# Kernel tuning notes

Measured on AMD Instinct MI355X. Metric: run time of the kernel, lower is better.

## Reference

```python
import jax, jax.numpy as jnp
import numpy as np
from jax import lax

# Matches init_kwargs: ops='co', window_size=[51, 25]
OPS = "co"
WINDOWS = [51, 25]


def _stage(x, k, mode):
    # Torch Conv1d(padding='same') zero-pads left=(k-1)//2, right=k//2, and the
    # identity-shift kernel bank + channel min/max is exactly a sliding-window
    # min/max over the zero-padded signal.
    left, right = (k - 1) // 2, k // 2
    xp = jnp.pad(x, ((0, 0), (0, 0), (left, right)))  # zeros, as in torch 'same'
    if mode == "max":  # dilation
        return lax.reduce_window(xp, float("-inf"), lax.max, (1, 1, k), (1, 1, 1), "VALID")
    # erosion
    return lax.reduce_window(xp, float("inf"), lax.min, (1, 1, k), (1, 1, 1), "VALID")


def _chain(x):
    # Per-channel python loop in the original is channel-independent; we batch it.
    for op, k in zip(OPS, WINDOWS):
        if op.lower() == "c":  # closing: dilation then erosion
            x = _stage(x, k, "max")
            x = _stage(x, k, "min")
        elif op.lower() == "o":  # opening: erosion then dilation
            x = _stage(x, k, "min")
            x = _stage(x, k, "max")
    return x


def setup_inputs() -> dict:
    key = jax.random.key(0)
    x = jax.random.normal(key, (16, 8, 262144), dtype=jnp.float32)  # [B, C, L]
    return {"x": x}


def reference(x):
    return _chain(x)
```

## Files before the change

### kernel.cpp

```cpp
#include <hip/hip_runtime.h>


#define L_ROW   262144
#define N_ROWS  128
#define BLOCK   256
#define E       32
#define EF4     8
#define T_VALID 7996
#define N_TILES 33
#define BUF_SLOTS 2048

__device__ __forceinline__ int swz(int s) { return s ^ ((s >> 3) & 7); }

template<bool MX>
__device__ __forceinline__ float mm(float a, float b) {
  return MX ? fmaxf(a, b) : fminf(a, b);
}

__device__ __forceinline__ void edge_zero(float* r, int goff, int tid, bool edge) {
  if (edge) {
    const int base = goff + tid * E;
#pragma unroll
    for (int i = 0; i < E; ++i)
      if ((unsigned)(base + i) >= (unsigned)L_ROW) r[i] = 0.0f;
  }
}

__device__ __forceinline__ void writeback(const float* r, float4* buf, int b4) {
#pragma unroll
  for (int j = 0; j < EF4; ++j)
    buf[swz(b4 + j)] = make_float4(r[4*j], r[4*j+1], r[4*j+2], r[4*j+3]);
  __syncthreads();
}

template<int K, bool MX>
__device__ __forceinline__ void stage_big(float* r, float4* buf, int tid,
                                          int goff, bool edge) {
  constexpr int BLEN = K - 33;
  constexpr int BN   = (BLEN + 2) / 4;
  const int b4 = tid * EF4;
  const int bh = min(b4, 2032 - BN);

  float4 v0 = buf[swz(bh + 8)];
  float a0 = v0.x, a1 = v0.y, a2 = v0.z, a3 = v0.w;
#pragma unroll
  for (int j = 1; j < BN - 1; ++j) {
    float4 v = buf[swz(bh + 8 + j)];
    a0 = mm<MX>(a0, v.x); a1 = mm<MX>(a1, v.y);
    a2 = mm<MX>(a2, v.z); a3 = mm<MX>(a3, v.w);
  }
  float4 vl = buf[swz(bh + 8 + BN - 1)];
  const float Base = mm<MX>(mm<MX>(mm<MX>(a0, a1), mm<MX>(a2, a3)),
                            mm<MX>(vl.x, vl.y));
  float T[34];
  T[0] = vl.z; T[1] = vl.w;
#pragma unroll
  for (int j = 0; j < 8; ++j) {
    float4 v = buf[swz(bh + 8 + BN + j)];
    T[2+4*j] = v.x; T[3+4*j] = v.y; T[4+4*j] = v.z; T[5+4*j] = v.w;
  }
  __syncthreads();

#pragma unroll
  for (int b = 0; b < 4; ++b)
#pragma unroll
    for (int i = 8*b + 6; i >= 8*b; --i) r[i] = mm<MX>(r[i], r[i+1]);
  const float S2 = r[24];
  const float S1 = mm<MX>(r[16], S2);
  const float S0 = mm<MX>(r[8],  S1);
#pragma unroll
  for (int i = 0;  i < 8;  ++i) r[i] = mm<MX>(r[i], S0);
#pragma unroll
  for (int i = 8;  i < 16; ++i) r[i] = mm<MX>(r[i], S1);
#pragma unroll
  for (int i = 16; i < 24; ++i) r[i] = mm<MX>(r[i], S2);

#pragma unroll
  for (int b = 0; b < 4; ++b)
#pragma unroll
    for (int i = 8*b + 1; i < 8*b + 8; ++i) T[i] = mm<MX>(T[i-1], T[i]);
  const float G0 = mm<MX>(Base, T[7]);
  const float G1 = mm<MX>(G0,   T[15]);
  const float G2 = mm<MX>(G1,   T[23]);

#pragma unroll
  for (int i = 0;  i < 8;  ++i) r[i] = mm<MX>(r[i], mm<MX>(Base, T[i]));
#pragma unroll
  for (int i = 8;  i < 16; ++i) r[i] = mm<MX>(r[i], mm<MX>(G0, T[i]));
#pragma unroll
  for (int i = 16; i < 24; ++i) r[i] = mm<MX>(r[i], mm<MX>(G1, T[i]));
#pragma unroll
  for (int i = 24; i < 32; ++i) r[i] = mm<MX>(r[i], mm<MX>(G2, T[i]));

  edge_zero(r, goff, tid, edge);
  writeback(r, buf, b4);
}

template<bool MX>
__device__ __forceinline__ void stage_25(float* r, float4* buf, int tid,
                                         int goff, bool edge) {
  const int b4 = tid * EF4;
  const int bh = min(b4, 2034);
  float h[24];
#pragma unroll
  for (int j = 0; j < 6; ++j) {
    float4 v = buf[swz(bh + 8 + j)];
    h[4*j] = v.x; h[4*j+1] = v.y; h[4*j+2] = v.z; h[4*j+3] = v.w;
  }
  __syncthreads();

  float t[8];
  t[0] = r[24];
#pragma unroll
  for (int i = 1; i < 8; ++i) t[i] = mm<MX>(t[i-1], r[24+i]);
#pragma unroll
  for (int i = 30; i >= 24; --i) r[i] = mm<MX>(r[i], r[i+1]);
#pragma unroll
  for (int i = 22; i >= 16; --i) r[i] = mm<MX>(r[i], r[i+1]);
  const float cA = r[16];
  const float A3 = r[24];
#pragma unroll
  for (int i = 16; i < 24; ++i) r[i] = mm<MX>(r[i], A3);
#pragma unroll
  for (int i = 14; i >= 8; --i) r[i] = mm<MX>(r[i], r[i+1]);
#pragma unroll
  for (int i = 6;  i >= 0; --i) r[i] = mm<MX>(r[i], r[i+1]);
  const float A1 = r[8];
#pragma unroll
  for (int i = 0; i < 8; ++i) r[i] = mm<MX>(r[i], A1);
#pragma unroll
  for (int b = 0; b < 3; ++b)
#pragma unroll
    for (int i = 8*b + 1; i < 8*b + 8; ++i) h[i] = mm<MX>(h[i-1], h[i]);
  const float aB  = h[7];
  const float cA2 = mm<MX>(cA, t[7]);
  const float G1  = mm<MX>(aB, h[15]);
#pragma unroll
  for (int i = 0;  i < 8;  ++i) r[i] = mm<MX>(r[i], mm<MX>(cA,  t[i]));
#pragma unroll
  for (int i = 8;  i < 16; ++i) r[i] = mm<MX>(r[i], mm<MX>(cA2, h[i-8]));
#pragma unroll
  for (int i = 16; i < 24; ++i) r[i] = mm<MX>(r[i], mm<MX>(aB,  h[i-8]));
#pragma unroll
  for (int i = 24; i < 32; ++i) r[i] = mm<MX>(r[i], mm<MX>(G1,  h[i-8]));

  edge_zero(r, goff, tid, edge);
  writeback(r, buf, b4);
}

__global__ __launch_bounds__(BLOCK)
void morph_co_kernel(const float* __restrict__ x, float* __restrict__ out) {
  __shared__ float4 buf[BUF_SLOTS];

  const int tid  = threadIdx.x;
  const int tile = blockIdx.x;
  const int row  = blockIdx.y;
  const float* __restrict__ xrow = x   + (size_t)row * L_ROW;
  float* __restrict__       orow = out + (size_t)row * L_ROW;

  const int c0 = tile * T_VALID - 76;
  const bool edge = (tile == 0) || (tile == N_TILES - 1);

  if (!edge) {
#if __has_builtin(__builtin_amdgcn_global_load_lds)
    const int w = tid >> 6, lane = tid & 63;
#pragma unroll
    for (int k = 0; k < 8; ++k) {
      const int q0 = k * 256 + w * 64;
      const float* g = xrow + c0 + 4 * swz(q0 + lane);
      __builtin_amdgcn_global_load_lds(
          (const __attribute__((address_space(1))) void*)g,
          (__attribute__((address_space(3))) void*)(&buf[q0]), 16, 0, 0);
    }
#else
#pragma unroll
    for (int k = 0; k < 8; ++k) {
      const int s = k * BLOCK + tid;
      buf[swz(s)] = *reinterpret_cast<const float4*>(xrow + c0 + 4 * s);
    }
#endif
  } else {
#pragma unroll
    for (int k = 0; k < 8; ++k) {
      const int s = k * BLOCK + tid;
      const int g = c0 + 4 * s;
      float4 v;
      if (g >= 0 && g + 3 < L_ROW) {
        v = *reinterpret_cast<const float4*>(xrow + g);
      } else {
        v.x = ((unsigned)(g + 0) < (unsigned)L_ROW) ? xrow[g + 0] : 0.0f;
        v.y = ((unsigned)(g + 1) < (unsigned)L_ROW) ? xrow[g + 1] : 0.0f;
        v.z = ((unsigned)(g + 2) < (unsigned)L_ROW) ? xrow[g + 2] : 0.0f;
        v.w = ((unsigned)(g + 3) < (unsigned)L_ROW) ? xrow[g + 3] : 0.0f;
      }
      buf[swz(s)] = v;
    }
  }
  __syncthreads();

  float r[E];
  {
    const int b4 = tid * EF4;
#pragma unroll
    for (int j = 0; j < EF4; ++j) {
      float4 v = buf[swz(b4 + j)];
      r[4*j] = v.x; r[4*j+1] = v.y; r[4*j+2] = v.z; r[4*j+3] = v.w;
    }
  }

  if (!edge) {
    stage_big<51, true >(r, buf, tid, 0, false);
    stage_big<75, false>(r, buf, tid, 0, false);
    stage_25 <     true>(r, buf, tid, 0, false);
  } else {
    stage_big<51, true >(r, buf, tid, c0 + 25, true);
    stage_big<51, false>(r, buf, tid, c0 + 50, true);
    stage_25 <    false>(r, buf, tid, c0 + 62, true);
    stage_25 <     true>(r, buf, tid, c0 + 74, true);
  }

  const int ob  = tile * T_VALID;
  const int nf4 = min(T_VALID, L_ROW - ob) >> 2;
  float4* og = reinterpret_cast<float4*>(orow + ob);
  for (int u = tid; u < nf4; u += BLOCK) {
    float4 a = buf[swz(u)];
    float4 b = buf[swz(u + 1)];
    og[u] = make_float4(a.z, a.w, b.x, b.y);
  }
}

extern "C" void kernel_launch(void* const* d_in, const int* in_sizes, int n_in,
                              void* d_out, int out_size, void* d_ws, size_t ws_size,
                              hipStream_t stream) {
  const float* x = (const float*)d_in[0];
  float* out = (float*)d_out;
  dim3 grid(N_TILES, N_ROWS);
  morph_co_kernel<<<grid, BLOCK, 0, stream>>>(x, out);
}
```

Measured before the change: 51.88 us.

## Give each wavefront its own tile to replace block barriers with wave-local fences

The kernel now splits each row into 135 smaller chunks and assigns one per wavefront, each with a private LDS slice. Because a wavefront's LDS accesses execute in order, the block-wide __syncthreads calls can become compiler-only memory fences and a vmcnt wait, removing barrier stalls between the morphology stages. The trade-off is more halo overlap, since each 1944-sample chunk re-reads about 76 samples on each side, which adds global traffic to an already bandwidth-heavy kernel. Interior outputs are written as unaligned float2 pairs, so neighbouring chunks write some boundary elements twice with identical values.

Measured after the change: 49.25 us, median of 2. -5.1%, faster.

```diff
diff --git a/kernel.cpp b/kernel.cpp
--- a/kernel.cpp
+++ b/kernel.cpp
@@ -6,20 +6,24 @@
 #define BLOCK   256
 #define E       32
 #define EF4     8
-#define T_VALID 7996
-#define N_TILES 33
-#define BUF_SLOTS 2048
+#define T_W     1944
+#define N_CHUNKS 135
+#define NSLOT   528
+
+typedef float f32x2 __attribute__((ext_vector_type(2)));
 
 __device__ __forceinline__ int swz(int s) { return s ^ ((s >> 3) & 7); }
+
+#define WFENCE() asm volatile("" ::: "memory")
 
 template<bool MX>
 __device__ __forceinline__ float mm(float a, float b) {
   return MX ? fmaxf(a, b) : fminf(a, b);
 }
 
-__device__ __forceinline__ void edge_zero(float* r, int goff, int tid, bool edge) {
+__device__ __forceinline__ void edge_zero(float* r, int goff, int lane, bool edge) {
   if (edge) {
-    const int base = goff + tid * E;
+    const int base = goff + lane * E;
 #pragma unroll
     for (int i = 0; i < E; ++i)
       if ((unsigned)(base + i) >= (unsigned)L_ROW) r[i] = 0.0f;
@@ -27,19 +31,20 @@
 }
 
 __device__ __forceinline__ void writeback(const float* r, float4* buf, int b4) {
+  WFENCE();
 #pragma unroll
   for (int j = 0; j < EF4; ++j)
     buf[swz(b4 + j)] = make_float4(r[4*j], r[4*j+1], r[4*j+2], r[4*j+3]);
-  __syncthreads();
+  WFENCE();
 }
 
 template<int K, bool MX>
-__device__ __forceinline__ void stage_big(float* r, float4* buf, int tid,
+__device__ __forceinline__ void stage_big(float* r, float4* buf, int lane,
                                           int goff, bool edge) {
   constexpr int BLEN = K - 33;
   constexpr int BN   = (BLEN + 2) / 4;
-  const int b4 = tid * EF4;
-  const int bh = min(b4, 2032 - BN);
+  const int b4 = lane * EF4;
+  const int bh = min(b4, NSLOT - 16 - BN);
 
   float4 v0 = buf[swz(bh + 8)];
   float a0 = v0.x, a1 = v0.y, a2 = v0.z, a3 = v0.w;
@@ -59,7 +64,6 @@
     float4 v = buf[swz(bh + 8 + BN + j)];
     T[2+4*j] = v.x; T[3+4*j] = v.y; T[4+4*j] = v.z; T[5+4*j] = v.w;
   }
-  __syncthreads();
 
 #pragma unroll
   for (int b = 0; b < 4; ++b)
@@ -92,22 +96,20 @@
 #pragma unroll
   for (int i = 24; i < 32; ++i) r[i] = mm<MX>(r[i], mm<MX>(G2, T[i]));
 
-  edge_zero(r, goff, tid, edge);
+  edge_zero(r, goff, lane, edge);
   writeback(r, buf, b4);
 }
 
 template<bool MX>
-__device__ __forceinline__ void stage_25(float* r, float4* buf, int tid,
+__device__ __forceinline__ void stage_25(float* r, float4* buf, int lane,
                                          int goff, bool edge) {
-  const int b4 = tid * EF4;
-  const int bh = min(b4, 2034);
+  const int b4 = lane * EF4;
   float h[24];
 #pragma unroll
   for (int j = 0; j < 6; ++j) {
-    float4 v = buf[swz(bh + 8 + j)];
+    float4 v = buf[swz(b4 + 8 + j)];
     h[4*j] = v.x; h[4*j+1] = v.y; h[4*j+2] = v.z; h[4*j+3] = v.w;
   }
-  __syncthreads();
 
   float t[8];
   t[0] = r[24];
@@ -144,88 +146,101 @@
 #pragma unroll
   for (int i = 24; i < 32; ++i) r[i] = mm<MX>(r[i], mm<MX>(G1,  h[i-8]));
 
-  edge_zero(r, goff, tid, edge);
+  edge_zero(r, goff, lane, edge);
   writeback(r, buf, b4);
 }
 
 __global__ __launch_bounds__(BLOCK)
 void morph_co_kernel(const float* __restrict__ x, float* __restrict__ out) {
-  __shared__ float4 buf[BUF_SLOTS];
-
-  const int tid  = threadIdx.x;
-  const int tile = blockIdx.x;
+  __shared__ float4 lds4[4 * NSLOT];
+
+  const int w    = threadIdx.x >> 6;
+  const int lane = threadIdx.x & 63;
+  const int c    = blockIdx.x * 4 + w;
   const int row  = blockIdx.y;
+  if (c >= N_CHUNKS) return;
+
+  float4* buf = lds4 + w * NSLOT;
   const float* __restrict__ xrow = x   + (size_t)row * L_ROW;
   float* __restrict__       orow = out + (size_t)row * L_ROW;
 
-  const int c0 = tile * T_VALID - 76;
-  const bool edge = (tile == 0) || (tile == N_TILES - 1);
+  const int ob = c * T_W;
+  const int c0 = ob - 76;
+  const bool edge = (c == 0) || (c == N_CHUNKS - 1);
+  const int b4 = lane * EF4;
+  float r[E];
 
   if (!edge) {
-#if __has_builtin(__builtin_amdgcn_global_load_lds)
-    const int w = tid >> 6, lane = tid & 63;
-#pragma unroll
-    for (int k = 0; k < 8; ++k) {
-      const int q0 = k * 256 + w * 64;
-      const float* g = xrow + c0 + 4 * swz(q0 + lane);
-      __builtin_amdgcn_global_load_lds(
-          (const __attribute__((address_space(1))) void*)g,
-          (__attribute__((address_space(3))) void*)(&buf[q0]), 16, 0, 0);
-    }
-#else
-#pragma unroll
-    for (int k = 0; k < 8; ++k) {
-      const int s = k * BLOCK + tid;
-      buf[swz(s)] = *reinterpret_cast<const float4*>(xrow + c0 + 4 * s);
-    }
-#endif
+#pragma unroll
+    for (int it = 0; it < 9; ++it) {
+      const int s = it * 64 + lane;
+      if (s < NSLOT) {
+        const float* g = xrow + c0 + 4 * swz(s);
+        __builtin_amdgcn_global_load_lds(
+            (const __attribute__((address_space(1))) void*)g,
+            (__attribute__((address_space(3))) void*)(&buf[it * 64]), 16, 0, 0);
+      }
+    }
+    asm volatile("s_waitcnt vmcnt(0)" ::: "memory");
   } else {
 #pragma unroll
-    for (int k = 0; k < 8; ++k) {
-      const int s = k * BLOCK + tid;
-      const int g = c0 + 4 * s;
-      float4 v;
-      if (g >= 0 && g + 3 < L_ROW) {
-        v = *reinterpret_cast<const float4*>(xrow + g);
-      } else {
+    for (int it = 0; it < 9; ++it) {
+      const int s = it * 64 + lane;
+      if (s < NSLOT) {
+        const int g = c0 + 4 * s;
+        float4 v;
         v.x = ((unsigned)(g + 0) < (unsigned)L_ROW) ? xrow[g + 0] : 0.0f;
         v.y = ((unsigned)(g + 1) < (unsigned)L_ROW) ? xrow[g + 1] : 0.0f;
         v.z = ((unsigned)(g + 2) < (unsigned)L_ROW) ? xrow[g + 2] : 0.0f;
         v.w = ((unsigned)(g + 3) < (unsigned)L_ROW) ? xrow[g + 3] : 0.0f;
-      }
-      buf[swz(s)] = v;
-    }
-  }
-  __syncthreads();
-
-  float r[E];
-  {
-    const int b4 = tid * EF4;
-#pragma unroll
-    for (int j = 0; j < EF4; ++j) {
-      float4 v = buf[swz(b4 + j)];
-      r[4*j] = v.x; r[4*j+1] = v.y; r[4*j+2] = v.z; r[4*j+3] = v.w;
-    }
+        buf[swz(s)] = v;
+      }
+    }
+    WFENCE();
+  }
+
+#pragma unroll
+  for (int j = 0; j < EF4; ++j) {
+    float4 v = buf[swz(b4 + j)];
+    r[4*j] = v.x; r[4*j+1] = v.y; r[4*j+2] = v.z; r[4*j+3] = v.w;
   }
 
   if (!edge) {
-    stage_big<51, true >(r, buf, tid, 0, false);
-    stage_big<75, false>(r, buf, tid, 0, false);
-    stage_25 <     true>(r, buf, tid, 0, false);
+    stage_big<51, true >(r, buf, lane, 0, false);
+    stage_big<75, false>(r, buf, lane, 0, false);
+    stage_25 <true >(r, buf, lane, 0, false);
   } else {
-    stage_big<51, true >(r, buf, tid, c0 + 25, true);
-    stage_big<51, false>(r, buf, tid, c0 + 50, true);
-    stage_25 <    false>(r, buf, tid, c0 + 62, true);
-    stage_25 <     true>(r, buf, tid, c0 + 74, true);
-  }
-
-  const int ob  = tile * T_VALID;
-  const int nf4 = min(T_VALID, L_ROW - ob) >> 2;
-  float4* og = reinterpret_cast<float4*>(orow + ob);
-  for (int u = tid; u < nf4; u += BLOCK) {
-    float4 a = buf[swz(u)];
-    float4 b = buf[swz(u + 1)];
-    og[u] = make_float4(a.z, a.w, b.x, b.y);
+    stage_big<51, true >(r, buf, lane, c0 + 25, true);
+    stage_big<51, false>(r, buf, lane, c0 + 50, true);
+    stage_25 <false>(r, buf, lane, c0 + 62, true);
+    stage_25 <true >(r, buf, lane, c0 + 74, true);
+  }
+
+  if (!edge) {
+#pragma unroll
+    for (int it = 0; it < 8; ++it) {
+      const int u = it * 64 + lane;
+      if (u < (T_W + 2) / 4 + 1) {
+        float4 v = buf[swz(u)];
+        float* p = orow + ob - 2 + 4 * u;
+        *reinterpret_cast<f32x2*>(p)     = f32x2{v.x, v.y};
+        *reinterpret_cast<f32x2*>(p + 2) = f32x2{v.z, v.w};
+      }
+    }
+  } else {
+    const int hi = min(ob + T_W, L_ROW);
+#pragma unroll
+    for (int it = 0; it < 8; ++it) {
+      const int u = it * 64 + lane;
+      if (u < (T_W + 2) / 4 + 1) {
+        float4 v = buf[swz(u)];
+        const int p = ob - 2 + 4 * u;
+        if (p     >= ob && p     < hi) orow[p]     = v.x;
+        if (p + 1 >= ob && p + 1 < hi) orow[p + 1] = v.y;
+        if (p + 2 >= ob && p + 2 < hi) orow[p + 2] = v.z;
+        if (p + 3 >= ob && p + 3 < hi) orow[p + 3] = v.w;
+      }
+    }
   }
 }
 
@@ -234,6 +249,6 @@
                               hipStream_t stream) {
   const float* x = (const float*)d_in[0];
   float* out = (float*)d_out;
-  dim3 grid(N_TILES, N_ROWS);
+  dim3 grid((N_CHUNKS + 3) / 4, N_ROWS);
   morph_co_kernel<<<grid, BLOCK, 0, stream>>>(x, out);
 }
```
